# Performance work log

Measured on AMD Instinct MI355X. Metric: run time of the kernel, lower is better.

## Reference

```python
import jax, jax.numpy as jnp
import numpy as np


def build_perm(total_channels, num_filters):
    """Replicates Net.permuted_new_perfect's nested slice-copies as one gather index."""
    ncpf = total_channels // num_filters
    tg = num_filters + ncpf * ((num_filters - 1) * num_filters) // 2
    perm = np.zeros(tg * ncpf, dtype=np.int32)
    count = 0
    for i in range(num_filters):
        for j in range(ncpf):
            if j == 0:
                for k in range(i, num_filters):
                    perm[count] = i * ncpf
                    perm[count + 1:count + ncpf] = np.arange(k * ncpf + 1, k * ncpf + ncpf)
                    count += ncpf
            else:
                for k in range(i + 1, num_filters):
                    perm[count + j] = i * ncpf + j
                    perm[count:count + j] = np.arange(k * ncpf, k * ncpf + j)
                    perm[count + j + 1:count + ncpf] = np.arange(k * ncpf + j + 1, k * ncpf + ncpf)
                    count += ncpf
    return jnp.asarray(perm)


PERM1 = build_perm(18, 6)    # 153 gathered channels, 51 groups of 3
PERM2 = build_perm(255, 5)   # 26265 gathered channels, 515 groups of 51


def dw_conv(x, w, b, groups):
    y = jax.lax.conv_general_dilated(
        x, w, window_strides=(1, 1), padding='VALID',
        dimension_numbers=('NCHW', 'OIHW', 'NCHW'),
        feature_group_count=groups)
    return y + b[None, :, None, None]


def maxpool2(x):
    return jax.lax.reduce_window(x, -jnp.inf, jax.lax.max,
                                 (1, 1, 2, 2), (1, 1, 2, 2), 'VALID')


def perm_groupconv(x, perm, w, b):
    # gather channels, then grouped 1x1 conv (each group: ncpf chans -> 1 chan)
    G, ncpf = w.shape
    B, _, H, W = x.shape
    xg = x[:, perm].reshape(B, G, ncpf, H, W)
    return jnp.einsum('bgchw,gc->bghw', xg, w) + b[None, :, None, None]


def setup_inputs() -> dict:
    key = jax.random.key(0)
    ks = jax.random.split(key, 17)
    s = 0.05
    return {
        'x': jax.random.normal(ks[0], (64, 3, 32, 32), jnp.float32),
        'dw1_w': jax.random.normal(ks[1], (18, 1, 5, 5), jnp.float32) * s,
        'dw1_b': jax.random.normal(ks[2], (18,), jnp.float32) * s,
        'pc1_w': jax.random.normal(ks[3], (51, 3), jnp.float32) * s,
        'pc1_b': jax.random.normal(ks[4], (51,), jnp.float32) * s,
        'dw2_w': jax.random.normal(ks[5], (255, 1, 5, 5), jnp.float32) * s,
        'dw2_b': jax.random.normal(ks[6], (255,), jnp.float32) * s,
        'pc2_w': jax.random.normal(ks[7], (515, 51), jnp.float32) * s,
        'pc2_b': jax.random.normal(ks[8], (515,), jnp.float32) * s,
        'oo_w': jax.random.normal(ks[9], (100, 515), jnp.float32) * s,
        'oo_b': jax.random.normal(ks[10], (100,), jnp.float32) * s,
        'fc1_w': jax.random.normal(ks[11], (120, 2500), jnp.float32) * s,
        'fc1_b': jax.random.normal(ks[12], (120,), jnp.float32) * s,
        'fc2_w': jax.random.normal(ks[13], (84, 120), jnp.float32) * s,
        'fc2_b': jax.random.normal(ks[14], (84,), jnp.float32) * s,
        'fc3_w': jax.random.normal(ks[15], (10, 84), jnp.float32) * s,
        'fc3_b': jax.random.normal(ks[16], (10,), jnp.float32) * s,
    }


def reference(x, dw1_w, dw1_b, pc1_w, pc1_b, dw2_w, dw2_b, pc2_w, pc2_b,
              oo_w, oo_b, fc1_w, fc1_b, fc2_w, fc2_b, fc3_w, fc3_b):
    h = dw_conv(x, dw1_w, dw1_b, groups=3)            # [B,18,28,28]
    h = perm_groupconv(h, PERM1, pc1_w, pc1_b)        # [B,51,28,28]
    h = maxpool2(jax.nn.relu(h))                      # [B,51,14,14]
    h = dw_conv(h, dw2_w, dw2_b, groups=51)           # [B,255,10,10]
    h = perm_groupconv(h, PERM2, pc2_w, pc2_b)        # [B,515,10,10]
    h = maxpool2(jax.nn.relu(h))                      # [B,515,5,5]
    h = jax.nn.relu(jnp.einsum('bchw,oc->bohw', h, oo_w) + oo_b[None, :, None, None])  # [B,100,5,5]
    h = h.reshape(h.shape[0], -1)                     # [B,2500]
    h = jax.nn.relu(h @ fc1_w.T + fc1_b)
    h = jax.nn.relu(h @ fc2_w.T + fc2_b)
    return h @ fc3_w.T + fc3_b                        # [B,10]
```

## Files before the change

kernel.cpp:

```cpp
#include <hip/hip_runtime.h>

static constexpr size_t OFF_XT = 0;
static constexpr size_t OFF_H1 = 786432;
static constexpr size_t OFF_H2 = 4399104;
static constexpr size_t OFF_H3 = 6958080;
static constexpr size_t OFF_H4 = 13486080;
static constexpr size_t OFF_H5 = 16782080;
static constexpr size_t OFF_H5B = OFF_H1;
static constexpr size_t OFF_H6 = 17422080;
static constexpr size_t OFF_H7 = 17452800;
static constexpr size_t OFF_M1 = 17474304;
static constexpr size_t OFF_M2 = 17475328;
static constexpr size_t OFF_W2 = 17484032;

struct Meta2 { int g; int special; float wj; int valid; };

__device__ inline void scan_ijk(int F, int ncpf, int g, int& oi, int& oj, int& ok) {
  int cnt = 0;
  for (int i = 0; i < F; ++i)
    for (int j = 0; j < ncpf; ++j) {
      int ks = (j == 0) ? i : i + 1;
      for (int k = ks; k < F; ++k) {
        if (cnt == g) { oi = i; oj = j; ok = k; return; }
        ++cnt;
      }
    }
  oi = 0; oj = 0; ok = 0;
}

__device__ inline float4 f4fma(float4 v, float w, float4 a) {
  a.x = fmaf(v.x, w, a.x); a.y = fmaf(v.y, w, a.y);
  a.z = fmaf(v.z, w, a.z); a.w = fmaf(v.w, w, a.w);
  return a;
}

__global__ void k0_setup(const float* __restrict__ x, const float* __restrict__ pc2_w,
                         float* ws) {
  int bx = blockIdx.x, tid = threadIdx.x;
  if (bx < 96) {
    __shared__ float t[64][33];
    int c = bx >> 5, y = bx & 31;
    for (int r = 0; r < 8; ++r) {
      int b = r * 8 + (tid >> 5), xx = tid & 31;
      t[b][xx] = x[((b * 3 + c) * 32 + y) * 32 + xx];
    }
    __syncthreads();
    float* xT = ws + OFF_XT / 4;
    for (int r = 0; r < 8; ++r) {
      int xx = r * 4 + (tid >> 6), b = tid & 63;
      xT[((c * 32 + y) * 32 + xx) * 64 + b] = t[b][xx];
    }
  } else if (bx == 96) {
    if (tid < 51) {
      int i, j, k; scan_ijk(6, 3, tid, i, j, k);
      int* src1 = (int*)((char*)ws + OFF_M1);
      for (int p = 0; p < 3; ++p)
        src1[tid * 4 + p] = (p == j) ? (i * 3 + j) : (k * 3 + p);
    }
  } else if (bx < 204) {
    int idx = (bx - 97) * 256 + tid;
    if (idx < 536 * 51) {
      int s = idx / 51, p = idx - s * 51;
      int k, base;
      if (s < 8)        { k = 0; base = 0; }
      else if (s < 64)  { k = 1; base = 8; }
      else if (s < 168) { k = 2; base = 64; }
      else if (s < 328) { k = 3; base = 168; }
      else              { k = 4; base = 328; }
      int id2 = s - base;
      int cnt = 51 * k + 1;
      Meta2* m2 = (Meta2*)((char*)ws + OFF_M2);
      float* W2 = (float*)((char*)ws + OFF_W2);
      if (id2 < cnt) {
        int i, j;
        if (id2 <= k) { i = id2; j = 0; }
        else { int t2 = id2 - (k + 1); i = t2 / 50; j = t2 - i * 50 + 1; }
        int off = 205 * i - 51 * ((i * (i - 1)) >> 1);
        int g = (j == 0) ? (off + (k - i))
                         : (off + (5 - i) + (j - 1) * (4 - i) + (k - i - 1));
        W2[s * 51 + p] = (p == j) ? 0.f : pc2_w[g * 51 + p];
        if (p == 0) {
          m2[s].g = g; m2[s].special = i * 51 + j;
          m2[s].wj = pc2_w[g * 51 + j]; m2[s].valid = 1;
        }
      } else {
        W2[s * 51 + p] = 0.f;
        if (p == 0) { m2[s].g = 0; m2[s].special = 0; m2[s].wj = 0.f; m2[s].valid = 0; }
      }
    }
  } else {
    int idx = (bx - 204) * 256 + tid;
    if (idx < 7680) (ws + OFF_H6 / 4)[idx] = 0.f;
  }
}

__global__ void __launch_bounds__(256) k1_dw1(const float* __restrict__ w,
                                              const float* __restrict__ bias, float* ws) {
  const float* xT = ws + OFF_XT / 4;
  float* h1 = ws + OFF_H1 / 4;
  int task = blockIdx.x * 4 + __builtin_amdgcn_readfirstlane(threadIdx.y);
  int l = threadIdx.x;
  int sub = l >> 4, b4 = (l & 15) * 4;
  int o = task / 196, rem = task - o * 196;
  int y = rem / 7, xo = (rem - y * 7) * 4 + sub;
  int c = o / 6;
  float bb = bias[o];
  float4 acc = {bb, bb, bb, bb};
  const float* src = xT + ((c * 32 + y) * 32 + xo) * 64 + b4;
  #pragma unroll
  for (int ky = 0; ky < 5; ++ky)
    #pragma unroll
    for (int kx = 0; kx < 5; ++kx) {
      float4 v = *(const float4*)(src + (ky * 32 + kx) * 64);
      acc = f4fma(v, w[o * 25 + ky * 5 + kx], acc);
    }
  *(float4*)(h1 + ((o * 28 + y) * 28 + xo) * 64 + b4) = acc;
}

__global__ void __launch_bounds__(256) k2_pc1(const float* __restrict__ w,
                                              const float* __restrict__ bias, float* ws) {
  const float* h1 = ws + OFF_H1 / 4;
  const int* src1 = (const int*)((const char*)ws + OFF_M1);
  float* h2 = ws + OFF_H2 / 4;
  int task = blockIdx.x * 4 + __builtin_amdgcn_readfirstlane(threadIdx.y);
  if (task >= 2499) return;
  int l = threadIdx.x;
  int sub = l >> 4, b4 = (l & 15) * 4;
  int g = task / 49, pc = task - g * 49;
  int pp = pc * 4 + sub;
  int py = pp / 14, px = pp - py * 14;
  int s0 = src1[g * 4 + 0], s1 = src1[g * 4 + 1], s2 = src1[g * 4 + 2];
  float w0 = w[g * 3 + 0], w1 = w[g * 3 + 1], w2 = w[g * 3 + 2], bb = bias[g];
  float4 m = {0.f, 0.f, 0.f, 0.f};
  #pragma unroll
  for (int dy = 0; dy < 2; ++dy)
    #pragma unroll
    for (int dx = 0; dx < 2; ++dx) {
      int y = py * 2 + dy, xx = px * 2 + dx;
      float4 a = {bb, bb, bb, bb};
      a = f4fma(*(const float4*)(h1 + ((s0 * 28 + y) * 28 + xx) * 64 + b4), w0, a);
      a = f4fma(*(const float4*)(h1 + ((s1 * 28 + y) * 28 + xx) * 64 + b4), w1, a);
      a = f4fma(*(const float4*)(h1 + ((s2 * 28 + y) * 28 + xx) * 64 + b4), w2, a);
      m.x = fmaxf(m.x, a.x); m.y = fmaxf(m.y, a.y);
      m.z = fmaxf(m.z, a.z); m.w = fmaxf(m.w, a.w);
    }
  *(float4*)(h2 + ((g * 14 + py) * 14 + px) * 64 + b4) = m;
}

__global__ void __launch_bounds__(256) k3_dw2(const float* __restrict__ w,
                                              const float* __restrict__ bias, float* ws) {
  const float* h2 = ws + OFF_H2 / 4;
  float* h3 = ws + OFF_H3 / 4;
  int task = blockIdx.x * 4 + __builtin_amdgcn_readfirstlane(threadIdx.y);
  if (task >= 6375) return;
  int l = threadIdx.x;
  int sub = l >> 4, b4 = (l & 15) * 4;
  int o = task / 25, pc = task - o * 25;
  int p = pc * 4 + sub;
  int y = p / 10, xo = p - y * 10;
  int c = o / 5;
  float bb = bias[o];
  float4 acc = {bb, bb, bb, bb};
  const float* src = h2 + ((c * 14 + y) * 14 + xo) * 64 + b4;
  #pragma unroll
  for (int ky = 0; ky < 5; ++ky)
    #pragma unroll
    for (int kx = 0; kx < 5; ++kx) {
      float4 v = *(const float4*)(src + (ky * 14 + kx) * 64);
      acc = f4fma(v, w[o * 25 + ky * 5 + kx], acc);
    }
  int py = y >> 1, dy = y & 1, px = xo >> 1, dx = xo & 1;
  *(float4*)(h3 + ((o * 25 + py * 5 + px) * 4 + dy * 2 + dx) * 64 + b4) = acc;
}

__global__ void __launch_bounds__(256) k4_pc2(const float* __restrict__ bias, float* ws) {
  const float* h3 = ws + OFF_H3 / 4;
  const float* W2 = (const float*)((const char*)ws + OFF_W2);
  const Meta2* m2 = (const Meta2*)((const char*)ws + OFF_M2);
  float* h4 = ws + OFF_H4 / 4;
  int b = threadIdx.x;
  int wv = __builtin_amdgcn_readfirstlane(threadIdx.y);
  int pyx = blockIdx.x;
  int chunk = blockIdx.y;
  int k;
  if (chunk < 1) k = 0; else if (chunk < 8) k = 1; else if (chunk < 21) k = 2;
  else if (chunk < 41) k = 3; else k = 4;
  int s0 = chunk * 8 + wv * 2;
  float acc[2][4];
  #pragma unroll
  for (int m = 0; m < 2; ++m)
    #pragma unroll
    for (int q = 0; q < 4; ++q) acc[m][q] = 0.f;
  const float* hb = h3 + (size_t)(k * 51 * 100 + pyx * 4) * 64 + b;
  const float* wr0 = W2 + (s0 + 0) * 51;
  const float* wr1 = W2 + (s0 + 1) * 51;
  for (int p = 0; p < 51; ++p) {
    float v0 = hb[p * 6400 + 0];
    float v1 = hb[p * 6400 + 64];
    float v2 = hb[p * 6400 + 128];
    float v3 = hb[p * 6400 + 192];
    float wa = wr0[p], wb = wr1[p];
    acc[0][0] = fmaf(v0, wa, acc[0][0]);
    acc[0][1] = fmaf(v1, wa, acc[0][1]);
    acc[0][2] = fmaf(v2, wa, acc[0][2]);
    acc[0][3] = fmaf(v3, wa, acc[0][3]);
    acc[1][0] = fmaf(v0, wb, acc[1][0]);
    acc[1][1] = fmaf(v1, wb, acc[1][1]);
    acc[1][2] = fmaf(v2, wb, acc[1][2]);
    acc[1][3] = fmaf(v3, wb, acc[1][3]);
  }
  #pragma unroll
  for (int m = 0; m < 2; ++m) {
    Meta2 mm = m2[s0 + m];
    if (!mm.valid) continue;
    const float* hs = h3 + (size_t)(mm.special * 100 + pyx * 4) * 64 + b;
    float bb = bias[mm.g];
    float r0 = fmaf(hs[0],   mm.wj, acc[m][0]) + bb;
    float r1 = fmaf(hs[64],  mm.wj, acc[m][1]) + bb;
    float r2 = fmaf(hs[128], mm.wj, acc[m][2]) + bb;
    float r3 = fmaf(hs[192], mm.wj, acc[m][3]) + bb;
    float r = fmaxf(fmaxf(r0, r1), fmaxf(r2, r3));
    h4[(mm.g * 25 + pyx) * 64 + b] = fmaxf(r, 0.f);
  }
}

__global__ void __launch_bounds__(256) k5_oo(const float* __restrict__ w, float* ws) {
  const float* h4 = ws + OFF_H4 / 4;
  __shared__ float red[4][4][64];
  int lane = threadIdx.x;
  int wv = __builtin_amdgcn_readfirstlane(threadIdx.y);
  int pyx = blockIdx.x, og = blockIdx.y, ks = blockIdx.z;
  int kb = ks ? 258 : 0;
  int kn = ks ? 257 : 258;
  int q = kn >> 2, r = kn & 3;
  int base = __builtin_amdgcn_readfirstlane(kb + wv * q + (wv < r ? wv : r));
  int n = q + (wv < r ? 1 : 0);
  const float* w0 = w + (og * 4 + 0) * 515;
  const float* w1 = w + (og * 4 + 1) * 515;
  const float* w2 = w + (og * 4 + 2) * 515;
  const float* w3 = w + (og * 4 + 3) * 515;
  const float* hp = h4 + pyx * 64 + lane;
  float a0 = 0.f, a1 = 0.f, a2 = 0.f, a3 = 0.f;
  #pragma unroll 4
  for (int i = 0; i < n; ++i) {
    int c = base + i;
    float v = hp[c * 1600];
    a0 = fmaf(v, w0[c], a0);
    a1 = fmaf(v, w1[c], a1);
    a2 = fmaf(v, w2[c], a2);
    a3 = fmaf(v, w3[c], a3);
  }
  red[wv][0][lane] = a0; red[wv][1][lane] = a1;
  red[wv][2][lane] = a2; red[wv][3][lane] = a3;
  __syncthreads();
  if (wv == 0) {
    float* h5p = ws + (ks ? OFF_H5B : OFF_H5) / 4;
    #pragma unroll
    for (int m = 0; m < 4; ++m) {
      float s = red[0][m][lane] + red[1][m][lane] + red[2][m][lane] + red[3][m][lane];
      h5p[((og * 4 + m) * 25 + pyx) * 64 + lane] = s;
    }
  }
}

__global__ void __launch_bounds__(256) k6_fc1(const float* __restrict__ w,
                                              const float* __restrict__ oo_b, float* ws) {
  const float* h5a = ws + OFF_H5 / 4;
  const float* h5b = ws + OFF_H5B / 4;
  float* h6 = ws + OFF_H6 / 4;
  __shared__ float red[4][4][64];
  int lane = threadIdx.x;
  int wv = __builtin_amdgcn_readfirstlane(threadIdx.y);
  int og = blockIdx.x, ks = blockIdx.y;
  int kb = ks * 156 + (ks < 4 ? ks : 4);
  int kn = 156 + (ks < 4 ? 1 : 0);
  int q = kn >> 2, r = kn & 3;
  int base = __builtin_amdgcn_readfirstlane(kb + wv * q + (wv < r ? wv : r));
  int n = q + (wv < r ? 1 : 0);
  const float* w0 = w + (og * 4 + 0) * 2500;
  const float* w1 = w + (og * 4 + 1) * 2500;
  const float* w2 = w + (og * 4 + 2) * 2500;
  const float* w3 = w + (og * 4 + 3) * 2500;
  float a0 = 0.f, a1 = 0.f, a2 = 0.f, a3 = 0.f;
  #pragma unroll 4
  for (int i = 0; i < n; ++i) {
    int k = base + i;
    float v = fmaxf(h5a[k * 64 + lane] + h5b[k * 64 + lane] + oo_b[k / 25], 0.f);
    a0 = fmaf(v, w0[k], a0);
    a1 = fmaf(v, w1[k], a1);
    a2 = fmaf(v, w2[k], a2);
    a3 = fmaf(v, w3[k], a3);
  }
  red[wv][0][lane] = a0; red[wv][1][lane] = a1;
  red[wv][2][lane] = a2; red[wv][3][lane] = a3;
  __syncthreads();
  if (wv == 0) {
    #pragma unroll
    for (int m = 0; m < 4; ++m) {
      float s = red[0][m][lane] + red[1][m][lane] + red[2][m][lane] + red[3][m][lane];
      atomicAdd(&h6[(og * 4 + m) * 64 + lane], s);
    }
  }
}

__global__ void __launch_bounds__(256) k7_fc2(const float* __restrict__ w,
                                              const float* __restrict__ fc1_b,
                                              const float* __restrict__ bias, float* ws) {
  const float* h6 = ws + OFF_H6 / 4;
  float* h7 = ws + OFF_H7 / 4;
  __shared__ float red[4][64];
  int lane = threadIdx.x & 63, wv = threadIdx.x >> 6;
  int o = blockIdx.x;
  float acc = 0.f;
  int i0 = wv * 30;
  #pragma unroll 5
  for (int i = i0; i < i0 + 30; ++i) {
    float v = fmaxf(h6[i * 64 + lane] + fc1_b[i], 0.f);
    acc = fmaf(v, w[o * 120 + i], acc);
  }
  red[wv][lane] = acc;
  __syncthreads();
  if (threadIdx.x < 64) {
    float s = red[0][lane] + red[1][lane] + red[2][lane] + red[3][lane] + bias[o];
    h7[o * 64 + lane] = fmaxf(s, 0.f);
  }
}

__global__ void __launch_bounds__(256) k8_fc3(const float* __restrict__ w,
                                              const float* __restrict__ bias,
                                              float* out, const float* ws) {
  const float* h7 = ws + OFF_H7 / 4;
  __shared__ float red[4][64];
  int lane = threadIdx.x & 63, wv = threadIdx.x >> 6;
  int o = blockIdx.x;
  float acc = 0.f;
  int i0 = wv * 21;
  #pragma unroll 7
  for (int i = i0; i < i0 + 21; ++i)
    acc = fmaf(h7[i * 64 + lane], w[o * 84 + i], acc);
  red[wv][lane] = acc;
  __syncthreads();
  if (threadIdx.x < 64) {
    float s = red[0][lane] + red[1][lane] + red[2][lane] + red[3][lane] + bias[o];
    out[lane * 10 + o] = s;
  }
}

extern "C" void kernel_launch(void* const* d_in, const int* in_sizes, int n_in,
                              void* d_out, int out_size, void* d_ws, size_t ws_size,
                              hipStream_t stream) {
  const float* x     = (const float*)d_in[0];
  const float* dw1_w = (const float*)d_in[1];
  const float* dw1_b = (const float*)d_in[2];
  const float* pc1_w = (const float*)d_in[3];
  const float* pc1_b = (const float*)d_in[4];
  const float* dw2_w = (const float*)d_in[5];
  const float* dw2_b = (const float*)d_in[6];
  const float* pc2_w = (const float*)d_in[7];
  const float* pc2_b = (const float*)d_in[8];
  const float* oo_w  = (const float*)d_in[9];
  const float* oo_b  = (const float*)d_in[10];
  const float* fc1_w = (const float*)d_in[11];
  const float* fc1_b = (const float*)d_in[12];
  const float* fc2_w = (const float*)d_in[13];
  const float* fc2_b = (const float*)d_in[14];
  const float* fc3_w = (const float*)d_in[15];
  const float* fc3_b = (const float*)d_in[16];
  float* ws = (float*)d_ws;
  float* out = (float*)d_out;

  hipLaunchKernelGGL(k0_setup, dim3(234), dim3(256), 0, stream, x, pc2_w, ws);
  hipLaunchKernelGGL(k1_dw1, dim3(882), dim3(64, 4), 0, stream, dw1_w, dw1_b, ws);
  hipLaunchKernelGGL(k2_pc1, dim3(625), dim3(64, 4), 0, stream, pc1_w, pc1_b, ws);
  hipLaunchKernelGGL(k3_dw2, dim3(1594), dim3(64, 4), 0, stream, dw2_w, dw2_b, ws);
  hipLaunchKernelGGL(k4_pc2, dim3(25, 67), dim3(64, 4), 0, stream, pc2_b, ws);
  hipLaunchKernelGGL(k5_oo, dim3(25, 25, 2), dim3(64, 4), 0, stream, oo_w, ws);
  hipLaunchKernelGGL(k6_fc1, dim3(30, 16), dim3(64, 4), 0, stream, fc1_w, oo_b, ws);
  hipLaunchKernelGGL(k7_fc2, dim3(84), dim3(256), 0, stream, fc2_w, fc1_b, fc2_b, ws);
  hipLaunchKernelGGL(k8_fc3, dim3(10), dim3(256), 0, stream, fc3_w, fc3_b, out, ws);
}
```

Measured before the change: 150.3 us.

## Fuse input transpose into dw1 conv and merge fc2/fc3 into one tail kernel

Drops the separate setup kernel that transposed x into workspace. The first depthwise conv now stages five input rows per block in shared memory and computes all six output channels of a group, with the metadata setup folded into extra blocks of the same launch. fc2 and fc3 are also merged into a single 10-block kernel where every block recomputes fc2 redundantly into shared memory. This removes two launches and a global round-trip, but the dw1 stage now runs on far fewer blocks and the tail repeats fc2 work ten times with heavy register use.

Measured after the change: 187.5 us. +24.8%, slower.

```diff
diff --git a/kernel.cpp b/kernel.cpp
--- a/kernel.cpp
+++ b/kernel.cpp
@@ -1,6 +1,5 @@
 #include <hip/hip_runtime.h>
 
-static constexpr size_t OFF_XT = 0;
 static constexpr size_t OFF_H1 = 786432;
 static constexpr size_t OFF_H2 = 4399104;
 static constexpr size_t OFF_H3 = 6958080;
@@ -8,7 +7,6 @@
 static constexpr size_t OFF_H5 = 16782080;
 static constexpr size_t OFF_H5B = OFF_H1;
 static constexpr size_t OFF_H6 = 17422080;
-static constexpr size_t OFF_H7 = 17452800;
 static constexpr size_t OFF_M1 = 17474304;
 static constexpr size_t OFF_M2 = 17475328;
 static constexpr size_t OFF_W2 = 17484032;
@@ -34,31 +32,57 @@
   return a;
 }
 
-__global__ void k0_setup(const float* __restrict__ x, const float* __restrict__ pc2_w,
-                         float* ws) {
-  int bx = blockIdx.x, tid = threadIdx.x;
-  if (bx < 96) {
-    __shared__ float t[64][33];
-    int c = bx >> 5, y = bx & 31;
-    for (int r = 0; r < 8; ++r) {
-      int b = r * 8 + (tid >> 5), xx = tid & 31;
-      t[b][xx] = x[((b * 3 + c) * 32 + y) * 32 + xx];
+__global__ void __launch_bounds__(256) k1_dw1(const float* __restrict__ x,
+                                              const float* __restrict__ w,
+                                              const float* __restrict__ bias,
+                                              const float* __restrict__ pc2_w,
+                                              float* ws) {
+  __shared__ float xl[5][32][65];
+  int bx = blockIdx.x;
+  int lane = threadIdx.x;
+  int tid = threadIdx.y * 64 + lane;
+  if (bx < 84) {
+    int c = bx / 28, y = bx - (bx / 28) * 28;
+    int b = tid >> 2, q = tid & 3;
+    #pragma unroll
+    for (int yy = 0; yy < 5; ++yy) {
+      const float* src = x + (((b * 3 + c) * 32 + (y + yy)) * 32 + q * 8);
+      float4 v0 = *(const float4*)(src);
+      float4 v1 = *(const float4*)(src + 4);
+      xl[yy][q * 8 + 0][b] = v0.x; xl[yy][q * 8 + 1][b] = v0.y;
+      xl[yy][q * 8 + 2][b] = v0.z; xl[yy][q * 8 + 3][b] = v0.w;
+      xl[yy][q * 8 + 4][b] = v1.x; xl[yy][q * 8 + 5][b] = v1.y;
+      xl[yy][q * 8 + 6][b] = v1.z; xl[yy][q * 8 + 7][b] = v1.w;
     }
     __syncthreads();
-    float* xT = ws + OFF_XT / 4;
-    for (int r = 0; r < 8; ++r) {
-      int xx = r * 4 + (tid >> 6), b = tid & 63;
-      xT[((c * 32 + y) * 32 + xx) * 64 + b] = t[b][xx];
-    }
-  } else if (bx == 96) {
+    float* h1 = ws + OFF_H1 / 4;
+    int wv = __builtin_amdgcn_readfirstlane(threadIdx.y);
+    for (int xo = wv * 7; xo < wv * 7 + 7; ++xo) {
+      float acc[6];
+      #pragma unroll
+      for (int m = 0; m < 6; ++m) acc[m] = bias[c * 6 + m];
+      #pragma unroll
+      for (int yy = 0; yy < 5; ++yy)
+        #pragma unroll
+        for (int kx = 0; kx < 5; ++kx) {
+          float v = xl[yy][xo + kx][lane];
+          #pragma unroll
+          for (int m = 0; m < 6; ++m)
+            acc[m] = fmaf(v, w[(c * 6 + m) * 25 + yy * 5 + kx], acc[m]);
+        }
+      #pragma unroll
+      for (int m = 0; m < 6; ++m)
+        h1[(((c * 6 + m) * 28 + y) * 28 + xo) * 64 + lane] = acc[m];
+    }
+  } else if (bx == 84) {
     if (tid < 51) {
       int i, j, k; scan_ijk(6, 3, tid, i, j, k);
       int* src1 = (int*)((char*)ws + OFF_M1);
       for (int p = 0; p < 3; ++p)
         src1[tid * 4 + p] = (p == j) ? (i * 3 + j) : (k * 3 + p);
     }
-  } else if (bx < 204) {
-    int idx = (bx - 97) * 256 + tid;
+  } else if (bx < 192) {
+    int idx = (bx - 85) * 256 + tid;
     if (idx < 536 * 51) {
       int s = idx / 51, p = idx - s * 51;
       int k, base;
@@ -89,32 +113,9 @@
       }
     }
   } else {
-    int idx = (bx - 204) * 256 + tid;
+    int idx = (bx - 192) * 256 + tid;
     if (idx < 7680) (ws + OFF_H6 / 4)[idx] = 0.f;
   }
-}
-
-__global__ void __launch_bounds__(256) k1_dw1(const float* __restrict__ w,
-                                              const float* __restrict__ bias, float* ws) {
-  const float* xT = ws + OFF_XT / 4;
-  float* h1 = ws + OFF_H1 / 4;
-  int task = blockIdx.x * 4 + __builtin_amdgcn_readfirstlane(threadIdx.y);
-  int l = threadIdx.x;
-  int sub = l >> 4, b4 = (l & 15) * 4;
-  int o = task / 196, rem = task - o * 196;
-  int y = rem / 7, xo = (rem - y * 7) * 4 + sub;
-  int c = o / 6;
-  float bb = bias[o];
-  float4 acc = {bb, bb, bb, bb};
-  const float* src = xT + ((c * 32 + y) * 32 + xo) * 64 + b4;
-  #pragma unroll
-  for (int ky = 0; ky < 5; ++ky)
-    #pragma unroll
-    for (int kx = 0; kx < 5; ++kx) {
-      float4 v = *(const float4*)(src + (ky * 32 + kx) * 64);
-      acc = f4fma(v, w[o * 25 + ky * 5 + kx], acc);
-    }
-  *(float4*)(h1 + ((o * 28 + y) * 28 + xo) * 64 + b4) = acc;
 }
 
 __global__ void __launch_bounds__(256) k2_pc1(const float* __restrict__ w,
@@ -303,47 +304,41 @@
   }
 }
 
-__global__ void __launch_bounds__(256) k7_fc2(const float* __restrict__ w,
-                                              const float* __restrict__ fc1_b,
-                                              const float* __restrict__ bias, float* ws) {
+__global__ void __launch_bounds__(256, 1) k7_tail(const float* __restrict__ w2,
+                                                  const float* __restrict__ fc1_b,
+                                                  const float* __restrict__ b2,
+                                                  const float* __restrict__ w3,
+                                                  const float* __restrict__ b3,
+                                                  float* out, const float* ws) {
   const float* h6 = ws + OFF_H6 / 4;
-  float* h7 = ws + OFF_H7 / 4;
+  __shared__ float h7s[84][64];
   __shared__ float red[4][64];
-  int lane = threadIdx.x & 63, wv = threadIdx.x >> 6;
-  int o = blockIdx.x;
+  int lane = threadIdx.x;
+  int wv = __builtin_amdgcn_readfirstlane(threadIdx.y);
+  int o3 = blockIdx.x;
+  float a6r[120];
+  #pragma unroll
+  for (int i = 0; i < 120; ++i)
+    a6r[i] = fmaxf(h6[i * 64 + lane] + fc1_b[i], 0.f);
+  for (int t = 0; t < 21; ++t) {
+    int o = wv * 21 + t;
+    float acc = b2[o];
+    #pragma unroll
+    for (int i = 0; i < 120; ++i)
+      acc = fmaf(a6r[i], w2[o * 120 + i], acc);
+    h7s[o][lane] = fmaxf(acc, 0.f);
+  }
+  __syncthreads();
   float acc = 0.f;
-  int i0 = wv * 30;
-  #pragma unroll 5
-  for (int i = i0; i < i0 + 30; ++i) {
-    float v = fmaxf(h6[i * 64 + lane] + fc1_b[i], 0.f);
-    acc = fmaf(v, w[o * 120 + i], acc);
+  #pragma unroll 7
+  for (int t = 0; t < 21; ++t) {
+    int i = wv * 21 + t;
+    acc = fmaf(h7s[i][lane], w3[o3 * 84 + i], acc);
   }
   red[wv][lane] = acc;
   __syncthreads();
-  if (threadIdx.x < 64) {
-    float s = red[0][lane] + red[1][lane] + red[2][lane] + red[3][lane] + bias[o];
-    h7[o * 64 + lane] = fmaxf(s, 0.f);
-  }
-}
-
-__global__ void __launch_bounds__(256) k8_fc3(const float* __restrict__ w,
-                                              const float* __restrict__ bias,
-                                              float* out, const float* ws) {
-  const float* h7 = ws + OFF_H7 / 4;
-  __shared__ float red[4][64];
-  int lane = threadIdx.x & 63, wv = threadIdx.x >> 6;
-  int o = blockIdx.x;
-  float acc = 0.f;
-  int i0 = wv * 21;
-  #pragma unroll 7
-  for (int i = i0; i < i0 + 21; ++i)
-    acc = fmaf(h7[i * 64 + lane], w[o * 84 + i], acc);
-  red[wv][lane] = acc;
-  __syncthreads();
-  if (threadIdx.x < 64) {
-    float s = red[0][lane] + red[1][lane] + red[2][lane] + red[3][lane] + bias[o];
-    out[lane * 10 + o] = s;
-  }
+  if (wv == 0)
+    out[lane * 10 + o3] = red[0][lane] + red[1][lane] + red[2][lane] + red[3][lane] + b3[o3];
 }
 
 extern "C" void kernel_launch(void* const* d_in, const int* in_sizes, int n_in,
@@ -369,13 +364,13 @@
   float* ws = (float*)d_ws;
   float* out = (float*)d_out;
 
-  hipLaunchKernelGGL(k0_setup, dim3(234), dim3(256), 0, stream, x, pc2_w, ws);
-  hipLaunchKernelGGL(k1_dw1, dim3(882), dim3(64, 4), 0, stream, dw1_w, dw1_b, ws);
+  hipLaunchKernelGGL(k1_dw1, dim3(222), dim3(64, 4), 0, stream,
+                     x, dw1_w, dw1_b, pc2_w, ws);
   hipLaunchKernelGGL(k2_pc1, dim3(625), dim3(64, 4), 0, stream, pc1_w, pc1_b, ws);
   hipLaunchKernelGGL(k3_dw2, dim3(1594), dim3(64, 4), 0, stream, dw2_w, dw2_b, ws);
   hipLaunchKernelGGL(k4_pc2, dim3(25, 67), dim3(64, 4), 0, stream, pc2_b, ws);
   hipLaunchKernelGGL(k5_oo, dim3(25, 25, 2), dim3(64, 4), 0, stream, oo_w, ws);
   hipLaunchKernelGGL(k6_fc1, dim3(30, 16), dim3(64, 4), 0, stream, fc1_w, oo_b, ws);
-  hipLaunchKernelGGL(k7_fc2, dim3(84), dim3(256), 0, stream, fc2_w, fc1_b, fc2_b, ws);
-  hipLaunchKernelGGL(k8_fc3, dim3(10), dim3(256), 0, stream, fc3_w, fc3_b, out, ws);
-}
+  hipLaunchKernelGGL(k7_tail, dim3(10), dim3(64, 4), 0, stream,
+                     fc2_w, fc1_b, fc2_b, fc3_w, fc3_b, out, ws);
+}
```
